# Kernel tuning notes

Hardware: AMD Instinct MI355X
Metric: run time of the kernel (lower is better)

## Reference

```python
import jax, jax.numpy as jnp
import numpy as np

B, S, HID = 2, 2048, 2048
NH, NKV, D = 16, 8, 128
QR, KR, VR = 6, 2, 2
WIN = 1024
CAP = 50.0
EPS = 1e-6
SCALE = D ** -0.5


def setup_inputs() -> dict:
    key = jax.random.key(0)
    ks = jax.random.split(key, 12)
    w = 0.02  # weight init scale for numerical sanity
    pos = jnp.arange(S, dtype=jnp.float32)[:, None]
    inv_freq = 1.0 / (10000.0 ** (jnp.arange(0, D, 2, dtype=jnp.float32) / D))  # [D/2]
    ang = pos * inv_freq[None, :]
    return {
        "hidden_states": jax.random.normal(ks[0], (B, S, HID), jnp.float32),
        "cos": jnp.cos(ang),
        "sin": jnp.sin(ang),
        "W_A_q": jax.random.normal(ks[1], (HID, NH * QR), jnp.float32) * w,
        "W_A_k": jax.random.normal(ks[2], (HID, NKV * KR), jnp.float32) * w,
        "W_A_v": jax.random.normal(ks[3], (HID, NKV * VR), jnp.float32) * w,
        "W_B_q": jax.random.normal(ks[4], (HID, QR * D), jnp.float32) * w,
        "W_B_k": jax.random.normal(ks[5], (HID, KR * D), jnp.float32) * w,
        "W_B_v": jax.random.normal(ks[6], (HID, VR * D), jnp.float32) * w,
        "o_proj_w": jax.random.normal(ks[7], (NH * D, HID), jnp.float32) * w,
        "qnorm_w": jnp.zeros((D,), jnp.float32),  # Gemma RMSNorm: scale = 1 + w
        "knorm_w": jnp.zeros((D,), jnp.float32),
        "k_cache_A": jnp.zeros((B, S, NKV, KR), jnp.float32),
        "k_cache_B": jnp.zeros((B, S, KR, D), jnp.float32),
        "v_cache_A": jnp.zeros((B, S, NKV, VR), jnp.float32),
        "v_cache_B": jnp.zeros((B, S, VR, D), jnp.float32),
        "kv_write_indices": jnp.arange(S, dtype=jnp.int32),
    }


def _rmsnorm(x, w):
    var = jnp.mean(x * x, axis=-1, keepdims=True)
    return x * jax.lax.rsqrt(var + EPS) * (1.0 + w)


def _rope(x, cos, sin):
    # x: [B,S,R,D]; first half = real, second half = imag (torch chunk layout)
    x1, x2 = x[..., : D // 2], x[..., D // 2 :]
    c = cos[None, :, None, :]
    s = sin[None, :, None, :]
    return jnp.concatenate([x1 * c - x2 * s, x1 * s + x2 * c], axis=-1)


def reference(hidden_states, cos, sin, W_A_q, W_A_k, W_A_v, W_B_q, W_B_k, W_B_v,
              o_proj_w, qnorm_w, knorm_w, k_cache_A, k_cache_B, v_cache_A,
              v_cache_B, kv_write_indices):
    hs = hidden_states
    A_q = (hs @ W_A_q).reshape(B, S, NH, QR)
    A_k = (hs @ W_A_k).reshape(B, S, NKV, KR)
    A_v = (hs @ W_A_v).reshape(B, S, NKV, VR)
    B_q = (hs @ W_B_q).reshape(B, S, QR, D)
    B_k = (hs @ W_B_k).reshape(B, S, KR, D)
    B_v = (hs @ W_B_v).reshape(B, S, VR, D)
    # qk-norm on B factors, then RoPE on B factors
    B_q = _rope(_rmsnorm(B_q, qnorm_w), cos, sin)
    B_k = _rope(_rmsnorm(B_k, knorm_w), cos, sin)
    # KV cache write (prefill: ctx_len = kv_write_indices[-1]+1 = S, static)
    k_cache_A = k_cache_A.at[:, kv_write_indices].set(A_k)
    k_cache_B = k_cache_B.at[:, kv_write_indices].set(B_k)
    v_cache_A = v_cache_A.at[:, kv_write_indices].set(A_v)
    v_cache_B = v_cache_B.at[:, kv_write_indices].set(B_v)
    ctx = S
    # materialize Q/K/V from rank-R factors
    Q = jnp.einsum('bshr,bsrd->bhsd', A_q, B_q) / QR          # [B,NH,S,D]
    Q = Q * SCALE
    K = jnp.einsum('bskr,bsrd->bskd', k_cache_A[:, :ctx], k_cache_B[:, :ctx]) / KR
    V = jnp.einsum('bskr,bsrd->bskd', v_cache_A[:, :ctx], v_cache_B[:, :ctx]) / VR
    K = jnp.repeat(K, NH // NKV, axis=2).transpose(0, 2, 1, 3)  # [B,NH,ctx,D]
    V = jnp.repeat(V, NH // NKV, axis=2).transpose(0, 2, 1, 3)
    scores = jnp.einsum('bhqd,bhkd->bhqk', Q, K)
    scores = jnp.tanh(scores / CAP) * CAP
    # causal + sliding window mask
    i = jnp.arange(S)[:, None]
    j = jnp.arange(ctx)[None, :]
    win = min(WIN, ctx)
    allowed = (j <= i) & (j > i - win)
    min_val = jnp.finfo(scores.dtype).min
    scores = jnp.where(allowed[None, None], scores, min_val)
    attn = jax.nn.softmax(scores.astype(jnp.float32), axis=-1).astype(Q.dtype)
    out = jnp.einsum('bhqk,bhkd->bhqd', attn, V)
    out = out.transpose(0, 2, 1, 3).reshape(B, S, NH * D)
    return out @ o_proj_w
```

## Files before the change

kernel.cpp:

```cpp
#include <hip/hip_runtime.h>
#include <math.h>

#define B_    2
#define S_    2048
#define HID_  2048
#define NH_   16
#define NKV_  8
#define D_    128
#define QR_   6
#define KR_   2
#define VR_   2
#define WIN_  1024
#define CAP_  50.0f
#define EPS_  1e-6f
#define SCALE_ 0.08838834764831845f

#define OFF_AQ 0
#define OFF_AK 96
#define OFF_AV 112
#define OFF_BQ 128
#define OFF_BK 896
#define OFF_BV 1152
#define NPACK  1408

using short8 = __attribute__((ext_vector_type(8))) short;
using f32x4  = __attribute__((ext_vector_type(4))) float;
using u16x4  = __attribute__((ext_vector_type(4))) unsigned short;

__device__ __forceinline__ unsigned short f2bf(float f) {
    union { float f; unsigned u; } v; v.f = f;
    unsigned r = v.u + 0x7FFFu + ((v.u >> 16) & 1u);
    return (unsigned short)(r >> 16);
}

__global__ __launch_bounds__(256) void cvt_f32_bf16(const float* __restrict__ src,
                                                    unsigned short* __restrict__ dst,
                                                    int n4) {
    int i = blockIdx.x * 256 + threadIdx.x;
    if (i < n4) {
        float4 v = ((const float4*)src)[i];
        u16x4 o;
        o[0] = f2bf(v.x); o[1] = f2bf(v.y); o[2] = f2bf(v.z); o[3] = f2bf(v.w);
        ((u16x4*)dst)[i] = o;
    }
}

__global__ __launch_bounds__(256) void transpose_pack(const float* __restrict__ src,
                                                      int K, int N,
                                                      unsigned short* __restrict__ dst,
                                                      int rowOff, int dstStride) {
    __shared__ float tile[32][33];
    const int k0 = blockIdx.y * 32, n0 = blockIdx.x * 32;
    const int tx = threadIdx.x & 31, ty = threadIdx.x >> 5;
#pragma unroll
    for (int i = ty; i < 32; i += 8) {
        const int k = k0 + i, n = n0 + tx;
        tile[i][tx] = (n < N) ? src[(size_t)k * N + n] : 0.f;
    }
    __syncthreads();
#pragma unroll
    for (int i = ty; i < 32; i += 8) {
        const int n = n0 + i, k = k0 + tx;
        if (n < N) dst[(size_t)(rowOff + n) * dstStride + k] = f2bf(tile[tx][i]);
    }
}

__global__ __launch_bounds__(256) void gemm_bf16(const unsigned short* __restrict__ A,
                                                 const unsigned short* __restrict__ Bt,
                                                 float* __restrict__ C,
                                                 int M, int N, int K) {
    __shared__ unsigned short As[4096];
    __shared__ unsigned short Bs[4096];

    const int t    = threadIdx.x;
    const int lane = t & 63, wid = t >> 6;
    const int wr = wid >> 1, wc = wid & 1;
    const int row0 = blockIdx.y * 128, col0 = blockIdx.x * 128;

    const int s0 = t, s1 = t + 256;
    const int r0 = s0 >> 2, cg0 = (s0 & 3) ^ ((r0 >> 1) & 3);
    const int r1 = s1 >> 2, cg1 = (s1 & 3) ^ ((r1 >> 1) & 3);
    const size_t aOff0 = (size_t)(row0 + r0) * K + cg0 * 8;
    const size_t aOff1 = (size_t)(row0 + r1) * K + cg1 * 8;
    const size_t bOff0 = (size_t)(col0 + r0) * K + cg0 * 8;
    const size_t bOff1 = (size_t)(col0 + r1) * K + cg1 * 8;

    f32x4 acc[4][4];
#pragma unroll
    for (int m = 0; m < 4; ++m)
#pragma unroll
        for (int n = 0; n < 4; ++n) { acc[m][n][0]=0.f; acc[m][n][1]=0.f; acc[m][n][2]=0.f; acc[m][n][3]=0.f; }

    const int l15 = lane & 15, kg = lane >> 4;
    const int rsw = ((l15 >> 1) & 3);
    int aoff[4], boff[4];
#pragma unroll
    for (int m = 0; m < 4; ++m) {
        const int ra = wr * 64 + m * 16 + l15;
        aoff[m] = ra * 32 + ((kg ^ rsw) * 8);
        const int rb = wc * 64 + m * 16 + l15;
        boff[m] = rb * 32 + ((kg ^ rsw) * 8);
    }

    for (int k0 = 0; k0 < K; k0 += 32) {
        const short8 av0 = *(const short8*)(A  + aOff0 + k0);
        const short8 av1 = *(const short8*)(A  + aOff1 + k0);
        const short8 bv0 = *(const short8*)(Bt + bOff0 + k0);
        const short8 bv1 = *(const short8*)(Bt + bOff1 + k0);
        __syncthreads();
        *(short8*)(As + s0 * 8) = av0;
        *(short8*)(As + s1 * 8) = av1;
        *(short8*)(Bs + s0 * 8) = bv0;
        *(short8*)(Bs + s1 * 8) = bv1;
        __syncthreads();
        short8 a[4], b[4];
#pragma unroll
        for (int m = 0; m < 4; ++m) a[m] = *(const short8*)(As + aoff[m]);
#pragma unroll
        for (int n = 0; n < 4; ++n) b[n] = *(const short8*)(Bs + boff[n]);
#pragma unroll
        for (int m = 0; m < 4; ++m)
#pragma unroll
            for (int n = 0; n < 4; ++n)
                acc[m][n] = __builtin_amdgcn_mfma_f32_16x16x32_bf16(a[m], b[n], acc[m][n], 0, 0, 0);
    }

#pragma unroll
    for (int m = 0; m < 4; ++m) {
#pragma unroll
        for (int n = 0; n < 4; ++n) {
            const int cc = col0 + wc * 64 + n * 16 + l15;
#pragma unroll
            for (int q = 0; q < 4; ++q) {
                const int rr = row0 + wr * 64 + m * 16 + kg * 4 + q;
                C[(size_t)rr * N + cc] = acc[m][n][q];
            }
        }
    }
}

__global__ __launch_bounds__(64) void norm_rope(float* __restrict__ Cp,
                                                int colOff, int R,
                                                const float* __restrict__ w,
                                                const float* __restrict__ cosT,
                                                const float* __restrict__ sinT) {
    const int blk = blockIdx.x;
    const int bs = blk / R, r = blk % R;
    const int s = bs % S_;
    const int l = threadIdx.x;
    float* v = Cp + (size_t)bs * NPACK + colOff + r * D_;
    float x1 = v[l];
    float x2 = v[l + 64];
    float ss = x1 * x1 + x2 * x2;
#pragma unroll
    for (int off = 32; off; off >>= 1) ss += __shfl_xor(ss, off);
    const float inv = 1.0f / sqrtf(ss * (1.0f / 128.0f) + EPS_);
    x1 *= inv * (1.0f + w[l]);
    x2 *= inv * (1.0f + w[l + 64]);
    const float c  = cosT[s * 64 + l];
    const float sn = sinT[s * 64 + l];
    v[l]      = x1 * c - x2 * sn;
    v[l + 64] = x1 * sn + x2 * c;
}

__global__ __launch_bounds__(256) void scatter_kernel(const float* __restrict__ Cp,
                                                      const int* __restrict__ idx,
                                                      float* __restrict__ eKA,
                                                      float* __restrict__ eKB,
                                                      float* __restrict__ eVA,
                                                      float* __restrict__ eVB) {
    const int bs = blockIdx.x;
    const int b  = bs / S_;
    const int s  = bs % S_;
    const int di = idx[s];
    const size_t dst = (size_t)b * S_ + di;
    const int t = threadIdx.x;
    const float* rowp = Cp + (size_t)bs * NPACK;
    if (t < 16) { eKA[dst * 16 + t] = rowp[OFF_AK + t]; eVA[dst * 16 + t] = rowp[OFF_AV + t]; }
    eKB[dst * 256 + t] = rowp[OFF_BK + t];
    eVB[dst * 256 + t] = rowp[OFF_BV + t];
}

__global__ __launch_bounds__(256) void assemble_kernel(const float* __restrict__ Cp,
                                                       const float* __restrict__ eKA,
                                                       const float* __restrict__ eKB,
                                                       const float* __restrict__ eVA,
                                                       const float* __restrict__ eVB,
                                                       unsigned short* __restrict__ Qo,
                                                       unsigned short* __restrict__ Ko,
                                                       unsigned short* __restrict__ Vo) {
    __shared__ float aq[96];
    __shared__ float bq[768];
    __shared__ float ka[16];
    __shared__ float kb[256];
    __shared__ float va[16];
    __shared__ float vb[256];

    const int bs = blockIdx.x;
    const int b  = bs / S_;
    const int s  = bs % S_;
    const int t  = threadIdx.x;
    const float* rowp = Cp + (size_t)bs * NPACK;

    if (t < 96) aq[t] = rowp[OFF_AQ + t];
    for (int i = t; i < 768; i += 256) bq[i] = rowp[OFF_BQ + i];
    if (t < 16) { ka[t] = eKA[(size_t)bs * 16 + t]; va[t] = eVA[(size_t)bs * 16 + t]; }
    kb[t] = eKB[(size_t)bs * 256 + t];
    vb[t] = eVB[(size_t)bs * 256 + t];
    __syncthreads();

    const float qf = SCALE_ / (float)QR_;
#pragma unroll
    for (int i = 0; i < 8; ++i) {
        const int o = t + 256 * i;
        const int h = o >> 7, d = o & 127;
        float acc = 0.f;
#pragma unroll
        for (int r = 0; r < QR_; ++r) acc = fmaf(aq[h * QR_ + r], bq[r * D_ + d], acc);
        Qo[(((size_t)b * NH_ + h) * S_ + s) * D_ + d] = f2bf(acc * qf);
    }
#pragma unroll
    for (int i = 0; i < 4; ++i) {
        const int o = t + 256 * i;
        const int g = o >> 7, d = o & 127;
        const float kk = 0.5f * (ka[g * 2 + 0] * kb[d] + ka[g * 2 + 1] * kb[D_ + d]);
        const float vv = 0.5f * (va[g * 2 + 0] * vb[d] + va[g * 2 + 1] * vb[D_ + d]);
        Ko[(((size_t)b * NKV_ + g) * S_ + s) * D_ + d] = f2bf(kk);
        Vo[(((size_t)b * NKV_ + g) * S_ + s) * D_ + d] = f2bf(vv);
    }
}

__global__ __launch_bounds__(256) void transpose_v(const unsigned short* __restrict__ Vn,
                                                   unsigned short* __restrict__ Vt) {
    __shared__ unsigned short ts[64][72];
    const int s0 = blockIdx.x * 64;
    const int d0 = blockIdx.y * 64;
    const int bk = blockIdx.z;
    const unsigned short* src = Vn + (size_t)bk * S_ * D_;
    unsigned short* dst = Vt + (size_t)bk * D_ * S_;
    const int t = threadIdx.x;
#pragma unroll
    for (int u = 0; u < 2; ++u) {
        const int sl = t + 256 * u;
        const int r = sl >> 3, g = sl & 7;
        *(short8*)&ts[r][g * 8] = *(const short8*)(src + (size_t)(s0 + r) * D_ + d0 + g * 8);
    }
    __syncthreads();
#pragma unroll
    for (int u = 0; u < 2; ++u) {
        const int sl = t + 256 * u;
        const int d = sl >> 3, g = sl & 7;
        short8 v;
#pragma unroll
        for (int e = 0; e < 8; ++e) v[e] = (short)ts[g * 8 + e][d];
        *(short8*)(dst + (size_t)(d0 + d) * S_ + s0 + g * 8) = v;
    }
}

__global__ __launch_bounds__(256) void attn_mfma(const unsigned short* __restrict__ Q,
                                                 const unsigned short* __restrict__ K,
                                                 const unsigned short* __restrict__ Vt,
                                                 unsigned short* __restrict__ O) {
    __shared__ unsigned short Ks[64 * 128];
    __shared__ unsigned short Vts[128 * 64];
    __shared__ unsigned short Ps[4][16 * 64];

    const int qt = blockIdx.x, h = blockIdx.y, b = blockIdx.z;
    const int kv = h >> 1;
    const int q0 = qt * 64;
    const int t = threadIdx.x;
    const int lane = t & 63, wid = t >> 6;
    const int l15 = lane & 15, kg = lane >> 4;

    const unsigned short* Qb = Q  + (size_t)(b * NH_  + h)  * S_ * D_;
    const unsigned short* Kb = K  + (size_t)(b * NKV_ + kv) * S_ * D_;
    const unsigned short* Vb = Vt + (size_t)(b * NKV_ + kv) * (size_t)D_ * S_;

    short8 qfrag[4];
#pragma unroll
    for (int c = 0; c < 4; ++c)
        qfrag[c] = *(const short8*)(Qb + (size_t)(q0 + wid * 16 + l15) * D_ + c * 32 + kg * 8);

    int ksSlot[4], vsSlot[4];
    size_t ksSrc[4], vsSrc[4];
#pragma unroll
    for (int u = 0; u < 4; ++u) {
        const int s = t + 256 * u;
        const int key = s >> 4, gp = s & 15, g = gp ^ (key & 7);
        ksSlot[u] = s * 8;
        ksSrc[u]  = (size_t)key * D_ + g * 8;
        const int d = s >> 3, gp2 = s & 7, g2 = gp2 ^ (d & 7);
        vsSlot[u] = s * 8;
        vsSrc[u]  = (size_t)d * S_ + g2 * 8;
    }

    const int kstart  = (q0 - (WIN_ - 1) > 0) ? (q0 - (WIN_ - 1)) : 0;
    const int k_begin = kstart & ~63;
    const int nt = (q0 + 64 - k_begin) >> 6;

    short8 kreg[4], vreg[4];
#pragma unroll
    for (int u = 0; u < 4; ++u) {
        kreg[u] = *(const short8*)(Kb + (size_t)k_begin * D_ + ksSrc[u]);
        vreg[u] = *(const short8*)(Vb + (size_t)k_begin + vsSrc[u]);
    }

    float m_run[4], l_run[4];
#pragma unroll
    for (int q = 0; q < 4; ++q) { m_run[q] = -INFINITY; l_run[q] = 0.f; }
    f32x4 oacc[8];
#pragma unroll
    for (int n = 0; n < 8; ++n) { oacc[n][0] = 0.f; oacc[n][1] = 0.f; oacc[n][2] = 0.f; oacc[n][3] = 0.f; }

    unsigned short* Pw = &Ps[wid][0];
    const int gi_base = q0 + wid * 16 + kg * 4;

    for (int ti = 0; ti < nt; ++ti) {
        const int k0 = k_begin + ti * 64;
        __syncthreads();
#pragma unroll
        for (int u = 0; u < 4; ++u) {
            *(short8*)(Ks  + ksSlot[u]) = kreg[u];
            *(short8*)(Vts + vsSlot[u]) = vreg[u];
        }
        __syncthreads();
        if (ti + 1 < nt) {
            const int k1 = k0 + 64;
#pragma unroll
            for (int u = 0; u < 4; ++u) {
                kreg[u] = *(const short8*)(Kb + (size_t)k1 * D_ + ksSrc[u]);
                vreg[u] = *(const short8*)(Vb + (size_t)k1 + vsSrc[u]);
            }
        }

        f32x4 sacc[4];
#pragma unroll
        for (int n = 0; n < 4; ++n) { sacc[n][0] = 0.f; sacc[n][1] = 0.f; sacc[n][2] = 0.f; sacc[n][3] = 0.f; }
#pragma unroll
        for (int c = 0; c < 4; ++c) {
#pragma unroll
            for (int n = 0; n < 4; ++n) {
                const short8 bf = *(const short8*)(Ks + (n * 16 + l15) * 128 + (((4 * c + kg) ^ (l15 & 7)) * 8));
                sacc[n] = __builtin_amdgcn_mfma_f32_16x16x32_bf16(qfrag[c], bf, sacc[n], 0, 0, 0);
            }
        }

        float p[4][4];
        float corr[4];
#pragma unroll
        for (int q = 0; q < 4; ++q) {
            const int gi = gi_base + q;
            float sv[4];
            float tm = -INFINITY;
#pragma unroll
            for (int n = 0; n < 4; ++n) {
                const float e = __expf(sacc[n][q] * (2.0f / CAP_));
                const float v = CAP_ - (2.0f * CAP_) / (e + 1.0f);
                const int gj = k0 + n * 16 + l15;
                const bool ok = (gj <= gi) && (gj > gi - WIN_);
                sv[n] = ok ? v : -INFINITY;
                tm = fmaxf(tm, sv[n]);
            }
            tm = fmaxf(tm, __shfl_xor(tm, 1));
            tm = fmaxf(tm, __shfl_xor(tm, 2));
            tm = fmaxf(tm, __shfl_xor(tm, 4));
            tm = fmaxf(tm, __shfl_xor(tm, 8));
            const float mnew  = fmaxf(m_run[q], tm);
            const float msafe = (mnew > -INFINITY) ? mnew : 0.f;
            corr[q] = __expf(m_run[q] - msafe);
            float ls = 0.f;
#pragma unroll
            for (int n = 0; n < 4; ++n) {
                const float pv = __expf(sv[n] - msafe);
                p[n][q] = pv;
                ls += pv;
            }
            ls += __shfl_xor(ls, 1);
            ls += __shfl_xor(ls, 2);
            ls += __shfl_xor(ls, 4);
            ls += __shfl_xor(ls, 8);
            l_run[q] = l_run[q] * corr[q] + ls;
            m_run[q] = mnew;
        }

#pragma unroll
        for (int n = 0; n < 4; ++n)
#pragma unroll
            for (int q = 0; q < 4; ++q) {
                const int r = kg * 4 + q;
                Pw[r * 64 + (((2 * n + (l15 >> 3)) ^ (r & 7)) * 8) + (l15 & 7)] = f2bf(p[n][q]);
            }

#pragma unroll
        for (int n = 0; n < 8; ++n) {
#pragma unroll
            for (int q = 0; q < 4; ++q) oacc[n][q] *= corr[q];
        }
#pragma unroll
        for (int c = 0; c < 2; ++c) {
            const short8 af = *(const short8*)(Pw + l15 * 64 + (((4 * c + kg) ^ (l15 & 7)) * 8));
#pragma unroll
            for (int n = 0; n < 8; ++n) {
                const int d = n * 16 + l15;
                const short8 bfv = *(const short8*)(Vts + d * 64 + (((4 * c + kg) ^ (d & 7)) * 8));
                oacc[n] = __builtin_amdgcn_mfma_f32_16x16x32_bf16(af, bfv, oacc[n], 0, 0, 0);
            }
        }
    }

#pragma unroll
    for (int q = 0; q < 4; ++q) {
        const float il = (l_run[q] > 0.f) ? 1.0f / l_run[q] : 0.f;
        unsigned short* orow = O + (size_t)(b * S_ + gi_base + q) * (NH_ * D_) + h * D_;
#pragma unroll
        for (int n = 0; n < 8; ++n)
            orow[n * 16 + l15] = f2bf(oacc[n][q] * il);
    }
}

extern "C" void kernel_launch(void* const* d_in, const int* in_sizes, int n_in,
                              void* d_out, int out_size, void* d_ws, size_t ws_size,
                              hipStream_t stream) {
    const float* hs   = (const float*)d_in[0];
    const float* cosT = (const float*)d_in[1];
    const float* sinT = (const float*)d_in[2];
    const float* WAq  = (const float*)d_in[3];
    const float* WAk  = (const float*)d_in[4];
    const float* WAv  = (const float*)d_in[5];
    const float* WBq  = (const float*)d_in[6];
    const float* WBk  = (const float*)d_in[7];
    const float* WBv  = (const float*)d_in[8];
    const float* Wo   = (const float*)d_in[9];
    const float* qnw  = (const float*)d_in[10];
    const float* knw  = (const float*)d_in[11];
    const float* kcA  = (const float*)d_in[12];
    const float* kcB  = (const float*)d_in[13];
    const float* vcA  = (const float*)d_in[14];
    const float* vcB  = (const float*)d_in[15];
    const int*   kidx = (const int*)d_in[16];
    float* out = (float*)d_out;

    const size_t MROW = (size_t)B_ * S_;
    char* w = (char*)d_ws;
    auto alloc = [&](size_t bytes) { char* r = w; w += (bytes + 255) & ~(size_t)255; return r; };

    unsigned short* hsbf = (unsigned short*)alloc(MROW * HID_ * 2);
    unsigned short* Wt   = (unsigned short*)alloc((size_t)NPACK * HID_ * 2);
    unsigned short* Wto  = (unsigned short*)alloc((size_t)HID_ * HID_ * 2);
    float* Cp  = (float*)alloc(MROW * NPACK * 4);
    float* eKA = (float*)alloc(MROW * 16 * 4);
    float* eKB = (float*)alloc(MROW * 256 * 4);
    float* eVA = (float*)alloc(MROW * 16 * 4);
    float* eVB = (float*)alloc(MROW * 256 * 4);
    unsigned short* Qbf = (unsigned short*)alloc((size_t)B_ * NH_  * S_ * D_ * 2);
    unsigned short* Kbf = (unsigned short*)alloc((size_t)B_ * NKV_ * S_ * D_ * 2);
    unsigned short* Vbf = (unsigned short*)alloc((size_t)B_ * NKV_ * S_ * D_ * 2);
    unsigned short* Vtb = (unsigned short*)alloc((size_t)B_ * NKV_ * S_ * D_ * 2);
    unsigned short* aObf = (unsigned short*)alloc(MROW * (NH_ * D_) * 2);

    const int M = (int)MROW;

    cvt_f32_bf16<<<(M * HID_ / 4 + 255) / 256, 256, 0, stream>>>(hs, hsbf, M * HID_ / 4);
    transpose_pack<<<dim3( 3, 64), 256, 0, stream>>>(WAq, HID_,   96, Wt, OFF_AQ, HID_);
    transpose_pack<<<dim3( 1, 64), 256, 0, stream>>>(WAk, HID_,   16, Wt, OFF_AK, HID_);
    transpose_pack<<<dim3( 1, 64), 256, 0, stream>>>(WAv, HID_,   16, Wt, OFF_AV, HID_);
    transpose_pack<<<dim3(24, 64), 256, 0, stream>>>(WBq, HID_,  768, Wt, OFF_BQ, HID_);
    transpose_pack<<<dim3( 8, 64), 256, 0, stream>>>(WBk, HID_,  256, Wt, OFF_BK, HID_);
    transpose_pack<<<dim3( 8, 64), 256, 0, stream>>>(WBv, HID_,  256, Wt, OFF_BV, HID_);
    transpose_pack<<<dim3(64, 64), 256, 0, stream>>>(Wo,  HID_, 2048, Wto, 0,     HID_);

    gemm_bf16<<<dim3(NPACK / 128, M / 128), 256, 0, stream>>>(hsbf, Wt, Cp, M, NPACK, HID_);

    norm_rope<<<M * QR_, 64, 0, stream>>>(Cp, OFF_BQ, QR_, qnw, cosT, sinT);
    norm_rope<<<M * KR_, 64, 0, stream>>>(Cp, OFF_BK, KR_, knw, cosT, sinT);

    hipMemcpyAsync(eKA, kcA, MROW * 16  * 4, hipMemcpyDeviceToDevice, stream);
    hipMemcpyAsync(eKB, kcB, MROW * 256 * 4, hipMemcpyDeviceToDevice, stream);
    hipMemcpyAsync(eVA, vcA, MROW * 16  * 4, hipMemcpyDeviceToDevice, stream);
    hipMemcpyAsync(eVB, vcB, MROW * 256 * 4, hipMemcpyDeviceToDevice, stream);
    scatter_kernel<<<M, 256, 0, stream>>>(Cp, kidx, eKA, eKB, eVA, eVB);

    assemble_kernel<<<M, 256, 0, stream>>>(Cp, eKA, eKB, eVA, eVB, Qbf, Kbf, Vbf);
    transpose_v<<<dim3(S_ / 64, D_ / 64, B_ * NKV_), 256, 0, stream>>>(Vbf, Vtb);

    attn_mfma<<<dim3(S_ / 64, NH_, B_), 256, 0, stream>>>(Qbf, Kbf, Vtb, aObf);

    gemm_bf16<<<dim3(HID_ / 128, M / 128), 256, 0, stream>>>(aObf, Wto, out, M, HID_, HID_);
}
```

Before: 443.6 us.

## Drop online-softmax max tracking using tanh cap bound; use LDS-direct loads in GEMM

The attention kernel drops the running-max and rescaling of online softmax. Softcapped scores are bounded by CAP (50), so exp(score) cannot overflow in fp32, and the row sum is now reduced across lanes once at the end instead of every tile. This removes per-tile shuffles, correction exps and accumulator rescales, at the cost of less headroom if scores approach the cap. Separately, the GEMM now stages tiles with global_load_lds direct-to-LDS loads and drops the XOR swizzle, which may introduce LDS bank conflicts on fragment reads.

```diff
diff --git a/kernel.cpp b/kernel.cpp
--- a/kernel.cpp
+++ b/kernel.cpp
@@ -33,6 +33,13 @@
     return (unsigned short)(r >> 16);
 }
 
+__device__ __forceinline__ void gload16(const unsigned short* g, unsigned short* l) {
+    __builtin_amdgcn_global_load_lds(
+        (const __attribute__((address_space(1))) unsigned int*)g,
+        (__attribute__((address_space(3))) unsigned int*)l,
+        16, 0, 0);
+}
+
 __global__ __launch_bounds__(256) void cvt_f32_bf16(const float* __restrict__ src,
                                                     unsigned short* __restrict__ dst,
                                                     int n4) {
@@ -77,13 +84,16 @@
     const int wr = wid >> 1, wc = wid & 1;
     const int row0 = blockIdx.y * 128, col0 = blockIdx.x * 128;
 
-    const int s0 = t, s1 = t + 256;
-    const int r0 = s0 >> 2, cg0 = (s0 & 3) ^ ((r0 >> 1) & 3);
-    const int r1 = s1 >> 2, cg1 = (s1 & 3) ^ ((r1 >> 1) & 3);
-    const size_t aOff0 = (size_t)(row0 + r0) * K + cg0 * 8;
-    const size_t aOff1 = (size_t)(row0 + r1) * K + cg1 * 8;
-    const size_t bOff0 = (size_t)(col0 + r0) * K + cg0 * 8;
-    const size_t bOff1 = (size_t)(col0 + r1) * K + cg1 * 8;
+    const int r0 = t >> 2, g0 = t & 3;
+    const int r1 = r0 + 64;
+    const unsigned short* aS0 = A  + (size_t)(row0 + r0) * K + g0 * 8;
+    const unsigned short* aS1 = A  + (size_t)(row0 + r1) * K + g0 * 8;
+    const unsigned short* bS0 = Bt + (size_t)(col0 + r0) * K + g0 * 8;
+    const unsigned short* bS1 = Bt + (size_t)(col0 + r1) * K + g0 * 8;
+    unsigned short* aD0 = As + wid * 512;
+    unsigned short* aD1 = As + 2048 + wid * 512;
+    unsigned short* bD0 = Bs + wid * 512;
+    unsigned short* bD1 = Bs + 2048 + wid * 512;
 
     f32x4 acc[4][4];
 #pragma unroll
@@ -92,26 +102,19 @@
         for (int n = 0; n < 4; ++n) { acc[m][n][0]=0.f; acc[m][n][1]=0.f; acc[m][n][2]=0.f; acc[m][n][3]=0.f; }
 
     const int l15 = lane & 15, kg = lane >> 4;
-    const int rsw = ((l15 >> 1) & 3);
     int aoff[4], boff[4];
 #pragma unroll
     for (int m = 0; m < 4; ++m) {
-        const int ra = wr * 64 + m * 16 + l15;
-        aoff[m] = ra * 32 + ((kg ^ rsw) * 8);
-        const int rb = wc * 64 + m * 16 + l15;
-        boff[m] = rb * 32 + ((kg ^ rsw) * 8);
+        aoff[m] = (wr * 64 + m * 16 + l15) * 32 + kg * 8;
+        boff[m] = (wc * 64 + m * 16 + l15) * 32 + kg * 8;
     }
 
     for (int k0 = 0; k0 < K; k0 += 32) {
-        const short8 av0 = *(const short8*)(A  + aOff0 + k0);
-        const short8 av1 = *(const short8*)(A  + aOff1 + k0);
-        const short8 bv0 = *(const short8*)(Bt + bOff0 + k0);
-        const short8 bv1 = *(const short8*)(Bt + bOff1 + k0);
         __syncthreads();
-        *(short8*)(As + s0 * 8) = av0;
-        *(short8*)(As + s1 * 8) = av1;
-        *(short8*)(Bs + s0 * 8) = bv0;
-        *(short8*)(Bs + s1 * 8) = bv1;
+        gload16(aS0 + k0, aD0);
+        gload16(aS1 + k0, aD1);
+        gload16(bS0 + k0, bD0);
+        gload16(bS1 + k0, bD1);
         __syncthreads();
         short8 a[4], b[4];
 #pragma unroll
@@ -305,9 +308,7 @@
         vreg[u] = *(const short8*)(Vb + (size_t)k_begin + vsSrc[u]);
     }
 
-    float m_run[4], l_run[4];
-#pragma unroll
-    for (int q = 0; q < 4; ++q) { m_run[q] = -INFINITY; l_run[q] = 0.f; }
+    float l_run[4] = {0.f, 0.f, 0.f, 0.f};
     f32x4 oacc[8];
 #pragma unroll
     for (int n = 0; n < 8; ++n) { oacc[n][0] = 0.f; oacc[n][1] = 0.f; oacc[n][2] = 0.f; oacc[n][3] = 0.f; }
@@ -346,41 +347,19 @@
         }
 
         float p[4][4];
-        float corr[4];
 #pragma unroll
         for (int q = 0; q < 4; ++q) {
             const int gi = gi_base + q;
-            float sv[4];
-            float tm = -INFINITY;
 #pragma unroll
             for (int n = 0; n < 4; ++n) {
-                const float e = __expf(sacc[n][q] * (2.0f / CAP_));
-                const float v = CAP_ - (2.0f * CAP_) / (e + 1.0f);
-                const int gj = k0 + n * 16 + l15;
-                const bool ok = (gj <= gi) && (gj > gi - WIN_);
-                sv[n] = ok ? v : -INFINITY;
-                tm = fmaxf(tm, sv[n]);
-            }
-            tm = fmaxf(tm, __shfl_xor(tm, 1));
-            tm = fmaxf(tm, __shfl_xor(tm, 2));
-            tm = fmaxf(tm, __shfl_xor(tm, 4));
-            tm = fmaxf(tm, __shfl_xor(tm, 8));
-            const float mnew  = fmaxf(m_run[q], tm);
-            const float msafe = (mnew > -INFINITY) ? mnew : 0.f;
-            corr[q] = __expf(m_run[q] - msafe);
-            float ls = 0.f;
-#pragma unroll
-            for (int n = 0; n < 4; ++n) {
-                const float pv = __expf(sv[n] - msafe);
+                const float e  = __expf(sacc[n][q] * (2.0f / CAP_));
+                const float r  = __builtin_amdgcn_rcpf(e + 1.0f);
+                const int  gj  = k0 + n * 16 + l15;
+                const bool ok  = (gj <= gi) && (gj > gi - WIN_);
+                const float pv = ok ? __expf(fmaf(-2.0f * CAP_, r, CAP_)) : 0.f;
                 p[n][q] = pv;
-                ls += pv;
-            }
-            ls += __shfl_xor(ls, 1);
-            ls += __shfl_xor(ls, 2);
-            ls += __shfl_xor(ls, 4);
-            ls += __shfl_xor(ls, 8);
-            l_run[q] = l_run[q] * corr[q] + ls;
-            m_run[q] = mnew;
+                l_run[q] += pv;
+            }
         }
 
 #pragma unroll
@@ -391,11 +370,6 @@
                 Pw[r * 64 + (((2 * n + (l15 >> 3)) ^ (r & 7)) * 8) + (l15 & 7)] = f2bf(p[n][q]);
             }
 
-#pragma unroll
-        for (int n = 0; n < 8; ++n) {
-#pragma unroll
-            for (int q = 0; q < 4; ++q) oacc[n][q] *= corr[q];
-        }
 #pragma unroll
         for (int c = 0; c < 2; ++c) {
             const short8 af = *(const short8*)(Pw + l15 * 64 + (((4 * c + kg) ^ (l15 & 7)) * 8));
@@ -410,7 +384,12 @@
 
 #pragma unroll
     for (int q = 0; q < 4; ++q) {
-        const float il = (l_run[q] > 0.f) ? 1.0f / l_run[q] : 0.f;
+        float ls = l_run[q];
+        ls += __shfl_xor(ls, 1);
+        ls += __shfl_xor(ls, 2);
+        ls += __shfl_xor(ls, 4);
+        ls += __shfl_xor(ls, 8);
+        const float il = (ls > 0.f) ? 1.0f / ls : 0.f;
         unsigned short* orow = O + (size_t)(b * S_ + gi_base + q) * (NH_ * D_) + h * D_;
 #pragma unroll
         for (int n = 0; n < 8; ++n)
```

Measured after the change: 395.7 us. -10.8%, faster.
